# Kernel optimization log

Measured on AMD Instinct MI355X. Metric: run time of the kernel, lower is better.

## Reference

```python
import jax, jax.numpy as jnp
import numpy as np

PAD = 7                 # init padding
T = 2 * PAD + 1         # T_side_dense = 15 shifts per axis
LAMDA = 1.0             # init lamda
EPS = 1e-16             # hardcoded epsilon in the torch loss body


def _joint_hist(x_out, x_tf_out):
    # Equivalent of F.conv2d(x_out.permute(1,0,2,3), weight=x_tf_out.permute(1,0,2,3), padding=PAD)
    # expressed as T*T shifted matmuls (correlation / cost-volume form).
    bn, k, h, w = x_out.shape
    A = jnp.transpose(x_out, (1, 0, 2, 3))      # (k, bn, h, w)  conv "input"
    B = jnp.transpose(x_tf_out, (1, 0, 2, 3))   # (k, bn, h, w)  conv "weight"
    A_pad = jnp.pad(A, ((0, 0), (0, 0), (PAD, PAD), (PAD, PAD)))

    def step(carry, s):
        dy, dx = s // T, s % T
        sl = jax.lax.dynamic_slice(A_pad, (0, 0, dy, dx), (k, bn, h, w))
        # p[n, o] at this shift = sum_{c,y,x} A_pad[n,c,y+dy,x+dx] * B[o,c,y,x]
        return carry, jnp.einsum('nchw,ochw->no', sl, B)

    _, p = jax.lax.scan(step, None, jnp.arange(T * T))
    # (T*T, k, k) -> (T, T, k, k); matches torch p_i_j.permute(2, 3, 0, 1)
    return p.reshape(T, T, k, k)


def reference(x_out, x_tf_out):
    p = _joint_hist(x_out, x_tf_out)
    # shift to positive; min is detached in torch -> stop_gradient
    p = p - jax.lax.stop_gradient(p.min()) + EPS
    # normalize per shift over the (k, k) joint
    p = p / p.sum(axis=(2, 3), keepdims=True)
    # symmetrize
    p = (p + jnp.swapaxes(p, 2, 3)) / 2.0
    p_i = p.sum(axis=2, keepdims=True)   # (T, T, 1, k) marginal (broadcasts like repeat)
    p_j = p.sum(axis=3, keepdims=True)   # (T, T, k, 1) marginal
    loss = (-p * (jnp.log(p + EPS)
                  - LAMDA * jnp.log(p_i + EPS)
                  - LAMDA * jnp.log(p_j + EPS))).sum() / (T * T)
    return loss


def setup_inputs() -> dict:
    key = jax.random.key(0)
    k1, k2 = jax.random.split(key)
    bn, k, h, w = 16, 10, 224, 224
    # simplex over axis=1 is asserted by the torch module -> use softmax
    x_out = jax.nn.softmax(jax.random.normal(k1, (bn, k, h, w), dtype=jnp.float32), axis=1)
    x_tf_out = jax.nn.softmax(jax.random.normal(k2, (bn, k, h, w), dtype=jnp.float32), axis=1)
    return {"x_out": x_out, "x_tf_out": x_tf_out}
```

## Files before the change

### kernel.cpp

```cpp
#include <hip/hip_runtime.h>
#include <stdint.h>
#include <math.h>


#define PADV 7
#define TS 15
#define KCLS 10
#define HH 224
#define WW 224
#define MD 160
#define NCELL (MD*MD)
#define NBLK 256
#define TY 14
#define AROW 240
#define BSTRIDE 232
#define BPH 240
#define LEPS 1e-16

typedef __attribute__((ext_vector_type(4))) float f32x4;
typedef __attribute__((ext_vector_type(8))) short bf16x8;

__device__ __forceinline__ unsigned short f2bf(float f) {
  union { float f; uint32_t u; } v; v.f = f;
  return (unsigned short)((v.u + 0x7FFFu + ((v.u >> 16) & 1u)) >> 16);
}

__device__ __forceinline__ void glds16(const unsigned short* g, unsigned short* l) {
  __builtin_amdgcn_global_load_lds(
      (const __attribute__((address_space(1))) unsigned int*)g,
      (__attribute__((address_space(3))) unsigned int*)l, 16, 0, 0);
}

__global__ __launch_bounds__(256)
void prep_b(const float* __restrict__ xt, unsigned short* __restrict__ bp) {
  const int idx   = blockIdx.x * 256 + threadIdx.x;
  const int rowid = idx / 29;
  const int chunk = idx - rowid * 29;
  const int x0    = chunk * 8;
  const int yy    = rowid % BPH;
  const int cls   = rowid / BPH;
  const int row   = yy - PADV;
  union { unsigned short h[8]; uint4 v; } out;
  if (row >= 0 && row < HH && x0 < WW) {
    const float* src = xt + ((size_t)cls * HH + row) * WW + x0;
#pragma unroll
    for (int j = 0; j < 8; ++j) out.h[j] = f2bf(src[j]);
  } else {
    out.v = make_uint4(0u, 0u, 0u, 0u);
  }
  *(uint4*)(bp + (size_t)rowid * BSTRIDE + x0) = out.v;
}

__global__ __launch_bounds__(640, 3)
void corr_gemm(const float* __restrict__ xo, const unsigned short* __restrict__ bpad,
               float* __restrict__ partials) {
  __shared__ __align__(16) unsigned short ldsA[2][KCLS * AROW];
  __shared__ __align__(16) unsigned short ldsB[KCLS * 16 * BSTRIDE];

  const int tid  = threadIdx.x;
  const int bid0 = blockIdx.x;
  const int bid  = (bid0 & 7) * 32 + (bid0 >> 3);
  const int b    = bid >> 4;
  const int y0   = (bid & 15) * TY;

  const int lane = tid & 63;
  const int wv   = tid >> 6;
  const int wm   = wv >> 1;
  const int wn   = wv & 1;
  const int quad = lane >> 4;
  const int l15  = lane & 15;

  f32x4 acc[2][5];
#pragma unroll
  for (int i = 0; i < 2; ++i)
#pragma unroll
    for (int j = 0; j < 5; ++j) acc[i][j] = (f32x4){0.f, 0.f, 0.f, 0.f};

  const float* Ab = xo + (size_t)b * KCLS * HH * WW;
  const unsigned short* Bb = bpad + (size_t)b * KCLS * BPH * BSTRIDE;

  for (int pr = wv; pr < 15 * KCLS; pr += 10) {
    const int r15  = pr / KCLS;
    const int o    = pr - r15 * KCLS;
    const int yy   = y0 + r15;
    const int slot = (y0 - PADV + r15) & 15;
    if (lane < 29)
      glds16(Bb + ((size_t)o * BPH + yy) * BSTRIDE + lane * 8,
             ldsB + (o * 16 + slot) * BSTRIDE);
  }

#pragma unroll
  for (int r = 0; r < 4; ++r) {
    const int t = tid + r * 640;
    if (t < KCLS * AROW) {
      const int n = t / AROW;
      const int i = t - n * AROW;
      const int x = i - PADV;
      float v = 0.f;
      if (x >= 0 && x < WW) v = Ab[((size_t)n * HH + y0) * WW + x];
      ldsA[0][t] = f2bf(v);
    }
  }
  __syncthreads();

  int cur = 0;
  float va[4];
  for (int s = 0; s < TY; ++s) {
    const int y = y0 + s;
    const bool more = (s + 1 < TY);

    if (more) {
      const int yy   = y + 8 + PADV;
      const int slot = (y + 8) & 15;
      if (lane < 29)
        glds16(Bb + ((size_t)wv * BPH + yy) * BSTRIDE + lane * 8,
               ldsB + (wv * 16 + slot) * BSTRIDE);
      const int yl = y + 1;
#pragma unroll
      for (int r = 0; r < 4; ++r) {
        const int t = tid + r * 640;
        float v = 0.f;
        if (t < KCLS * AROW) {
          const int n = t / AROW;
          const int i = t - n * AROW;
          const int x = i - PADV;
          if (x >= 0 && x < WW) v = Ab[((size_t)n * HH + yl) * WW + x];
        }
        va[r] = v;
      }
    }

    const unsigned short* la = ldsA[cur];
#pragma unroll 1
    for (int xc = 0; xc < 7; ++xc) {
      const int x0 = xc * 32;
      bf16x8 afrag[2], bfrag[5];
      const int e0 = x0 + quad * 8 + l15;
      const int q  = e0 >> 1;
      const int sh = (e0 & 1) << 4;
#pragma unroll
      for (int mi = 0; mi < 2; ++mi) {
        const int tm = wm * 2 + mi;
        const uint32_t* pa = (const uint32_t*)la + tm * (AROW / 2);
        uint32_t w0 = pa[q], w1 = pa[q + 1], w2 = pa[q + 2],
                 w3 = pa[q + 3], w4 = pa[q + 4];
        union { uint32_t u[4]; bf16x8 v; } cv;
        cv.u[0] = __builtin_amdgcn_alignbit(w1, w0, sh);
        cv.u[1] = __builtin_amdgcn_alignbit(w2, w1, sh);
        cv.u[2] = __builtin_amdgcn_alignbit(w3, w2, sh);
        cv.u[3] = __builtin_amdgcn_alignbit(w4, w3, sh);
        afrag[mi] = cv.v;
      }
      const int slot = (y + PADV - l15) & 15;
#pragma unroll
      for (int ni = 0; ni < 5; ++ni) {
        const int to = wn * 5 + ni;
        bfrag[ni] = *(const bf16x8*)(ldsB + (to * 16 + slot) * BSTRIDE + x0 + quad * 8);
      }
#pragma unroll
      for (int mi = 0; mi < 2; ++mi)
#pragma unroll
        for (int ni = 0; ni < 5; ++ni)
          acc[mi][ni] = __builtin_amdgcn_mfma_f32_16x16x32_bf16(
              afrag[mi], bfrag[ni], acc[mi][ni], 0, 0, 0);
    }

    if (more) {
      unsigned short* an = ldsA[cur ^ 1];
#pragma unroll
      for (int r = 0; r < 4; ++r) {
        const int t = tid + r * 640;
        if (t < KCLS * AROW) an[t] = f2bf(va[r]);
      }
      __syncthreads();
      cur ^= 1;
    }
  }

  float* outp = partials + (size_t)bid * NCELL;
#pragma unroll
  for (int mi = 0; mi < 2; ++mi)
#pragma unroll
    for (int ni = 0; ni < 5; ++ni) {
      const int mrow = (wm * 2 + mi) * 16 + quad * 4;
      const int ncol = (wn * 5 + ni) * 16 + l15;
#pragma unroll
      for (int r = 0; r < 4; ++r)
        outp[(size_t)(mrow + r) * MD + ncol] = acc[mi][ni][r];
    }
}

__global__ __launch_bounds__(256)
void reduce_stage1(const float* __restrict__ partials, float* __restrict__ stage2) {
  const int c  = (blockIdx.x % 100) * 256 + threadIdx.x;
  const int pg = blockIdx.x / 100;
  const float* base = partials + (size_t)pg * 32 * NCELL + c;
  float s0 = 0.f, s1 = 0.f, s2 = 0.f, s3 = 0.f;
  for (int p = 0; p < 32; p += 4) {
    s0 += base[(size_t)(p + 0) * NCELL];
    s1 += base[(size_t)(p + 1) * NCELL];
    s2 += base[(size_t)(p + 2) * NCELL];
    s3 += base[(size_t)(p + 3) * NCELL];
  }
  stage2[(size_t)pg * NCELL + c] = (s0 + s1) + (s2 + s3);
}

__global__ __launch_bounds__(256)
void reduce_final(const float* __restrict__ stage2, float* __restrict__ Cout,
                  float* __restrict__ mins, float* __restrict__ dout) {
  const int c = blockIdx.x * 256 + threadIdx.x;
  if (blockIdx.x == 0 && threadIdx.x == 0) dout[0] = 0.f;
  double s = 0.0;
#pragma unroll
  for (int pg = 0; pg < 8; ++pg) s += (double)stage2[(size_t)pg * NCELL + c];
  const float sf = (float)s;
  Cout[c] = sf;
  const int m  = c / MD;
  const int nn = c - m * MD;
  const bool valid = ((m & 15) < TS) && ((nn & 15) < TS);
  __shared__ float red[256];
  red[threadIdx.x] = valid ? sf : 3.4e38f;
  __syncthreads();
  for (int st = 128; st > 0; st >>= 1) {
    if (threadIdx.x < st)
      red[threadIdx.x] = fminf(red[threadIdx.x], red[threadIdx.x + st]);
    __syncthreads();
  }
  if (threadIdx.x == 0) mins[blockIdx.x] = red[0];
}

__global__ __launch_bounds__(128)
void loss_kernel(const float* __restrict__ Cmat, const float* __restrict__ mins,
                 float* __restrict__ dout) {
  const int s   = blockIdx.x;
  const int dy  = s / TS;
  const int dx  = s - dy * TS;
  const int tid = threadIdx.x;
  __shared__ float fm[128];
  __shared__ double q[100];
  __shared__ double sym[100];
  __shared__ double pi[10], pj[10];
  __shared__ double red[128];

  fm[tid] = (tid < 100) ? mins[tid] : 3.4e38f;
  __syncthreads();
  for (int st = 64; st > 0; st >>= 1) {
    if (tid < st) fm[tid] = fminf(fm[tid], fm[tid + st]);
    __syncthreads();
  }
  const double minv = (double)fm[0];
  __syncthreads();

  if (tid < 100) {
    const int n = tid / 10, o = tid - (tid / 10) * 10;
    const double v = (double)Cmat[(size_t)(n * 16 + dx) * MD + (o * 16 + dy)];
    q[tid] = v - minv + LEPS;
  }
  __syncthreads();
  red[tid] = (tid < 100) ? q[tid] : 0.0;
  __syncthreads();
  for (int st = 64; st > 0; st >>= 1) {
    if (tid < st) red[tid] += red[tid + st];
    __syncthreads();
  }
  const double Z = red[0];
  __syncthreads();
  if (tid < 100) {
    const int n = tid / 10, o = tid - (tid / 10) * 10;
    sym[tid] = (q[n * 10 + o] + q[o * 10 + n]) * 0.5 / Z;
  }
  __syncthreads();
  if (tid < 10) {
    double a = 0.0, bsum = 0.0;
    for (int n2 = 0; n2 < 10; ++n2) {
      a    += sym[n2 * 10 + tid];
      bsum += sym[tid * 10 + n2];
    }
    pi[tid] = a;
    pj[tid] = bsum;
  }
  __syncthreads();
  double term = 0.0;
  if (tid < 100) {
    const int n = tid / 10, o = tid - (tid / 10) * 10;
    const double sp = sym[tid];
    term = -sp * (log(sp + LEPS) - log(pi[o] + LEPS) - log(pj[n] + LEPS));
  }
  red[tid] = term;
  __syncthreads();
  for (int st = 64; st > 0; st >>= 1) {
    if (tid < st) red[tid] += red[tid + st];
    __syncthreads();
  }
  if (tid == 0) atomicAdd(dout, (float)(red[0] / (double)(TS * TS)));
}

extern "C" void kernel_launch(void* const* d_in, const int* in_sizes, int n_in,
                              void* d_out, int out_size, void* d_ws, size_t ws_size,
                              hipStream_t stream) {
  const float* xo = (const float*)d_in[0];
  const float* xt = (const float*)d_in[1];
  float* ws       = (float*)d_ws;

  float* partials = ws;
  float* stage2   = partials + (size_t)NBLK * NCELL;
  float* Cmat     = stage2 + (size_t)8 * NCELL;
  float* mins     = Cmat + NCELL;
  unsigned short* bpad = (unsigned short*)(mins + 128);
  float* out      = (float*)d_out;

  hipLaunchKernelGGL(prep_b,        dim3(4350), dim3(256), 0, stream, xt, bpad);
  hipLaunchKernelGGL(corr_gemm,     dim3(NBLK), dim3(640), 0, stream, xo, bpad, partials);
  hipLaunchKernelGGL(reduce_stage1, dim3(800),  dim3(256), 0, stream, partials, stage2);
  hipLaunchKernelGGL(reduce_final,  dim3(100),  dim3(256), 0, stream, stage2, Cmat, mins, out);
  hipLaunchKernelGGL(loss_kernel,   dim3(225),  dim3(128), 0, stream, Cmat, mins, out);
}
```

Before: 155.3 us.

## Store A rows as eight pre-shifted bf16 planes for aligned fragment loads

The A tile in LDS becomes eight copies of each padded row, each shifted by one element, so every MFMA A-fragment is a single aligned 16-byte LDS read. This replaces the five 32-bit reads plus four alignbit ops per fragment. The global A load also changes from scalar per-element reads by all threads to float4 vector loads by 300 threads that pack to bf16 and write all planes. LDS use for A grows about eightfold, which may reduce occupancy or raise LDS write traffic per row.

```diff
diff --git a/kernel.cpp b/kernel.cpp
--- a/kernel.cpp
+++ b/kernel.cpp
@@ -12,9 +12,10 @@
 #define NCELL (MD*MD)
 #define NBLK 256
 #define TY 14
-#define AROW 240
 #define BSTRIDE 232
 #define BPH 240
+#define PLANEE 2408
+#define ABUFE (8*PLANEE)
 #define LEPS 1e-16
 
 typedef __attribute__((ext_vector_type(4))) float f32x4;
@@ -23,12 +24,36 @@
 __device__ __forceinline__ unsigned short f2bf(float f) {
   union { float f; uint32_t u; } v; v.f = f;
   return (unsigned short)((v.u + 0x7FFFu + ((v.u >> 16) & 1u)) >> 16);
+}
+
+__device__ __forceinline__ uint32_t pack2bf(float a, float b) {
+  return (uint32_t)f2bf(a) | ((uint32_t)f2bf(b) << 16);
 }
 
 __device__ __forceinline__ void glds16(const unsigned short* g, unsigned short* l) {
   __builtin_amdgcn_global_load_lds(
       (const __attribute__((address_space(1))) unsigned int*)g,
       (__attribute__((address_space(3))) unsigned int*)l, 16, 0, 0);
+}
+
+__device__ __forceinline__ void plane_write(const f32x4 f[4], unsigned short* awr) {
+  uint32_t w[8];
+#pragma unroll
+  for (int k = 0; k < 8; ++k)
+    w[k] = pack2bf(f[k >> 1][(k & 1) * 2], f[k >> 1][(k & 1) * 2 + 1]);
+#pragma unroll
+  for (int c = 0; c < 8; ++c) {
+    union { uint32_t u[4]; uint4 v; } o;
+    if (c & 1) {
+#pragma unroll
+      for (int j = 0; j < 4; ++j) o.u[j] = w[j + (c + 1) / 2];
+    } else {
+#pragma unroll
+      for (int j = 0; j < 4; ++j)
+        o.u[j] = __builtin_amdgcn_alignbit(w[j + 1 + c / 2], w[j + c / 2], 16);
+    }
+    *(uint4*)(awr + c * PLANEE) = o.v;
+  }
 }
 
 __global__ __launch_bounds__(256)
@@ -54,7 +79,7 @@
 __global__ __launch_bounds__(640, 3)
 void corr_gemm(const float* __restrict__ xo, const unsigned short* __restrict__ bpad,
                float* __restrict__ partials) {
-  __shared__ __align__(16) unsigned short ldsA[2][KCLS * AROW];
+  __shared__ __align__(16) unsigned short ldsA8[2 * ABUFE];
   __shared__ __align__(16) unsigned short ldsB[KCLS * 16 * BSTRIDE];
 
   const int tid  = threadIdx.x;
@@ -78,6 +103,16 @@
 
   const float* Ab = xo + (size_t)b * KCLS * HH * WW;
   const unsigned short* Bb = bpad + (size_t)b * KCLS * BPH * BSTRIDE;
+
+  const bool aw  = tid < 300;
+  const int an   = aw ? tid / 30 : 0;
+  const int atp  = aw ? tid - (tid / 30) * 30 : 0;
+  const int axb  = atp * 8 - 8;
+  bool gv[4];
+#pragma unroll
+  for (int g = 0; g < 4; ++g)
+    gv[g] = aw && (axb + 4 * g >= 0) && (axb + 4 * g + 4 <= WW);
+  unsigned short* const awr0 = ldsA8 + an * 240 + atp * 8;
 
   for (int pr = wv; pr < 15 * KCLS; pr += 10) {
     const int r15  = pr / KCLS;
@@ -89,22 +124,19 @@
              ldsB + (o * 16 + slot) * BSTRIDE);
   }
 
-#pragma unroll
-  for (int r = 0; r < 4; ++r) {
-    const int t = tid + r * 640;
-    if (t < KCLS * AROW) {
-      const int n = t / AROW;
-      const int i = t - n * AROW;
-      const int x = i - PADV;
-      float v = 0.f;
-      if (x >= 0 && x < WW) v = Ab[((size_t)n * HH + y0) * WW + x];
-      ldsA[0][t] = f2bf(v);
-    }
-  }
+  f32x4 f[4];
+  {
+    const float* src = Ab + ((size_t)an * HH + y0) * WW + axb;
+#pragma unroll
+    for (int g = 0; g < 4; ++g) {
+      f[g] = (f32x4){0.f, 0.f, 0.f, 0.f};
+      if (gv[g]) f[g] = *(const f32x4*)(src + 4 * g);
+    }
+  }
+  if (aw) plane_write(f, awr0);
   __syncthreads();
 
   int cur = 0;
-  float va[4];
   for (int s = 0; s < TY; ++s) {
     const int y = y0 + s;
     const bool more = (s + 1 < TY);
@@ -115,47 +147,28 @@
       if (lane < 29)
         glds16(Bb + ((size_t)wv * BPH + yy) * BSTRIDE + lane * 8,
                ldsB + (wv * 16 + slot) * BSTRIDE);
-      const int yl = y + 1;
-#pragma unroll
-      for (int r = 0; r < 4; ++r) {
-        const int t = tid + r * 640;
-        float v = 0.f;
-        if (t < KCLS * AROW) {
-          const int n = t / AROW;
-          const int i = t - n * AROW;
-          const int x = i - PADV;
-          if (x >= 0 && x < WW) v = Ab[((size_t)n * HH + yl) * WW + x];
-        }
-        va[r] = v;
+      const float* src = Ab + ((size_t)an * HH + (y + 1)) * WW + axb;
+#pragma unroll
+      for (int g = 0; g < 4; ++g) {
+        f[g] = (f32x4){0.f, 0.f, 0.f, 0.f};
+        if (gv[g]) f[g] = *(const f32x4*)(src + 4 * g);
       }
     }
 
-    const unsigned short* la = ldsA[cur];
+    const unsigned short* paB = ldsA8 + cur * ABUFE + (l15 & 7) * PLANEE + (l15 & 8);
+    const int slotB = (y + PADV - l15) & 15;
+
 #pragma unroll 1
     for (int xc = 0; xc < 7; ++xc) {
       const int x0 = xc * 32;
       bf16x8 afrag[2], bfrag[5];
-      const int e0 = x0 + quad * 8 + l15;
-      const int q  = e0 >> 1;
-      const int sh = (e0 & 1) << 4;
-#pragma unroll
-      for (int mi = 0; mi < 2; ++mi) {
-        const int tm = wm * 2 + mi;
-        const uint32_t* pa = (const uint32_t*)la + tm * (AROW / 2);
-        uint32_t w0 = pa[q], w1 = pa[q + 1], w2 = pa[q + 2],
-                 w3 = pa[q + 3], w4 = pa[q + 4];
-        union { uint32_t u[4]; bf16x8 v; } cv;
-        cv.u[0] = __builtin_amdgcn_alignbit(w1, w0, sh);
-        cv.u[1] = __builtin_amdgcn_alignbit(w2, w1, sh);
-        cv.u[2] = __builtin_amdgcn_alignbit(w3, w2, sh);
-        cv.u[3] = __builtin_amdgcn_alignbit(w4, w3, sh);
-        afrag[mi] = cv.v;
-      }
-      const int slot = (y + PADV - l15) & 15;
+#pragma unroll
+      for (int mi = 0; mi < 2; ++mi)
+        afrag[mi] = *(const bf16x8*)(paB + (wm * 2 + mi) * 240 + x0 + quad * 8);
 #pragma unroll
       for (int ni = 0; ni < 5; ++ni) {
         const int to = wn * 5 + ni;
-        bfrag[ni] = *(const bf16x8*)(ldsB + (to * 16 + slot) * BSTRIDE + x0 + quad * 8);
+        bfrag[ni] = *(const bf16x8*)(ldsB + (to * 16 + slotB) * BSTRIDE + x0 + quad * 8);
       }
 #pragma unroll
       for (int mi = 0; mi < 2; ++mi)
@@ -166,12 +179,7 @@
     }
 
     if (more) {
-      unsigned short* an = ldsA[cur ^ 1];
-#pragma unroll
-      for (int r = 0; r < 4; ++r) {
-        const int t = tid + r * 640;
-        if (t < KCLS * AROW) an[t] = f2bf(va[r]);
-      }
+      if (aw) plane_write(f, awr0 + (cur ^ 1) * ABUFE);
       __syncthreads();
       cur ^= 1;
     }
```

New measurement: 150.9 us. 1.03x faster.
